# Kernel optimization log

Measured on AMD Instinct MI355X. Metric: run time of the kernel, lower is better.

The kernel has to match this reference:

```python
import jax, jax.numpy as jnp
import numpy as np

H, D_IN, E = 8, 512, 512
KD = VD = E // H  # 64
B, N = 16, 1024  # batch, graph_size (== n_query, self-attention)
NEG_INF = -1e30  # stands in for -np.inf; identical post-softmax, NaN-safe


def _uniform(key, shape, stdv):
    return jax.random.uniform(key, shape, jnp.float32, -stdv, stdv)


def setup_inputs() -> dict:
    key = jax.random.key(0)
    kq, km, k1, k2, k3, k4 = jax.random.split(key, 6)
    q = jax.random.normal(kq, (B, N, D_IN), jnp.float32)
    mask = jax.random.bernoulli(km, 0.15, (B, N, N))
    W_query = _uniform(k1, (H, D_IN, KD), 1.0 / np.sqrt(KD))
    W_key = _uniform(k2, (H, D_IN, KD), 1.0 / np.sqrt(KD))
    W_val = _uniform(k3, (H, D_IN, VD), 1.0 / np.sqrt(VD))
    W_out = _uniform(k4, (H, VD, E), 1.0 / np.sqrt(E))
    return {"q": q, "mask": mask, "W_query": W_query, "W_key": W_key,
            "W_val": W_val, "W_out": W_out}


def reference(q, mask, W_query, W_key, W_val, W_out):
    # h = q (self-attention path of the module)
    kd = W_query.shape[-1]
    scale = 1.0 / np.sqrt(kd).astype(np.float32)
    Q = jnp.einsum('bni,hik->hbnk', q, W_query)   # (H,B,N,kd)
    K = jnp.einsum('bgi,hik->hbgk', q, W_key)     # (H,B,G,kd)
    V = jnp.einsum('bgi,hiv->hbgv', q, W_val)     # (H,B,G,vd)
    compat = scale * jnp.einsum('hbnk,hbgk->hbng', Q, K)  # (H,B,N,G)
    m = mask[None]                                 # (1,B,N,G) broadcasts over heads
    compat = jnp.where(m, NEG_INF, compat)
    attn = jax.nn.softmax(compat, axis=-1)
    attn = jnp.where(m, 0.0, attn)
    heads = jnp.einsum('hbng,hbgv->hbnv', attn, V)
    out = jnp.einsum('hbnv,hve->bne', heads, W_out)  # (B,N,E)
    return out
```

## Files before the change

kernel.cpp:

```cpp
#include <hip/hip_runtime.h>
#include <hip/hip_bf16.h>

#define HH 8
#define DIN 512
#define HD 64
#define BB 16
#define NN 1024
#define LOG2E 1.44269504f

typedef float f32x4 __attribute__((ext_vector_type(4)));
typedef short s16x8 __attribute__((ext_vector_type(8)));
typedef unsigned int u32x4 __attribute__((ext_vector_type(4)));
typedef __bf16 bf16x8 __attribute__((ext_vector_type(8)));

__device__ __forceinline__ short f2bf(float f) {
  union { float f; unsigned u; } v; v.f = f;
  unsigned r = v.u + 0x7FFFu + ((v.u >> 16) & 1u);
  return (short)(r >> 16);
}

__device__ __forceinline__ unsigned cvtpk(float lo, float hi) {
  unsigned r;
  asm("v_cvt_pk_bf16_f32 %0, %1, %2" : "=v"(r) : "v"(lo), "v"(hi));
  return r;
}

__device__ __forceinline__ float exp2v(float x) {
  float r;
  asm("v_exp_f32 %0, %1" : "=v"(r) : "v"(x));
  return r;
}

__device__ __forceinline__ f32x4 mfma16(s16x8 a, s16x8 b, f32x4 c) {
  return __builtin_amdgcn_mfma_f32_16x16x32_bf16(
      __builtin_bit_cast(bf16x8, a), __builtin_bit_cast(bf16x8, b), c, 0, 0, 0);
}

#define GLDS16(gsrc, ldst)                                          \
  __builtin_amdgcn_global_load_lds(                                 \
      (const __attribute__((address_space(1))) void*)(gsrc),        \
      (__attribute__((address_space(3))) void*)(ldst), 16, 0, 0)

__global__ void k_detect(const unsigned char* __restrict__ m, int* __restrict__ flag) {
  const int t = threadIdx.x;
  const int nz = (m[4 * t + 1] != 0);
  unsigned long long b = __ballot(nz);
  __shared__ unsigned int anyv;
  if (t == 0) anyv = 0u;
  __syncthreads();
  if ((t & 63) == 0 && b) atomicOr(&anyv, 1u);
  __syncthreads();
  if (t == 0) flag[0] = (int)anyv;
}

__global__ void k_prep(const void* __restrict__ mk, const int* __restrict__ flag,
                       unsigned char* __restrict__ mwords,
                       const float* __restrict__ q, short* __restrict__ qbf,
                       const float* __restrict__ Wq, const float* __restrict__ Wk,
                       const float* __restrict__ Wv, const float* __restrict__ Wo,
                       short* __restrict__ Wt, short* __restrict__ Wot) {
  __shared__ float t[64][65];
  const int blk = blockIdx.x;
  if (blk < 8192) {
    const int i = blk * 256 + threadIdx.x;
    unsigned bits = 0;
    if (flag[0]) {
      const unsigned long long v = ((const unsigned long long*)mk)[i];
#pragma unroll
      for (int j = 0; j < 8; ++j)
        bits |= (((v >> (8 * j)) & 0xFFull) ? 1u : 0u) << j;
    } else {
      const uint4 a = ((const uint4*)mk)[2 * i];
      const uint4 c = ((const uint4*)mk)[2 * i + 1];
      bits = (a.x ? 1u : 0u) | (a.y ? 2u : 0u) | (a.z ? 4u : 0u) | (a.w ? 8u : 0u) |
             (c.x ? 16u : 0u) | (c.y ? 32u : 0u) | (c.z ? 64u : 0u) | (c.w ? 128u : 0u);
    }
    mwords[i] = (unsigned char)bits;
  } else if (blk < 12288) {
    const int i = (blk - 8192) * 256 + threadIdx.x;
    const float4* s4 = (const float4*)q;
    float4 a = s4[2 * i], c = s4[2 * i + 1];
    s16x8 o;
    o[0] = f2bf(a.x); o[1] = f2bf(a.y); o[2] = f2bf(a.z); o[3] = f2bf(a.w);
    o[4] = f2bf(c.x); o[5] = f2bf(c.y); o[6] = f2bf(c.z); o[7] = f2bf(c.w);
    ((s16x8*)qbf)[i] = o;
  } else {
    const int idx = blk - 12288;
    const float* in;
    short* op;
    int N, k0, n0;
    float scale = 1.0f;
    if (idx < 192) {
      const int mat = idx >> 6, rem = idx & 63, head = rem >> 3, kb = rem & 7;
      in = (mat == 0 ? Wq : (mat == 1 ? Wk : Wv)) + head * (DIN * HD);
      op = Wt + (size_t)(mat * 8 + head) * (HD * DIN);
      N = 64; k0 = kb * 64; n0 = 0;
      if (mat == 0) scale = 0.125f * LOG2E;
    } else {
      const int t2 = idx - 192;
      in = Wo; op = Wot;
      N = 512; k0 = (t2 >> 3) * 64; n0 = (t2 & 7) * 64;
    }
    const int tx = threadIdx.x & 63, ty = threadIdx.x >> 6;
#pragma unroll
    for (int i = 0; i < 16; ++i) {
      const int k = ty + i * 4;
      t[k][tx] = in[(size_t)(k0 + k) * N + n0 + tx];
    }
    __syncthreads();
#pragma unroll
    for (int i = 0; i < 16; ++i) {
      const int n = ty + i * 4;
      op[(size_t)(n0 + n) * DIN + k0 + tx] = f2bf(t[tx][n] * scale);
    }
  }
}

template <int MODE>
__global__ __launch_bounds__(256, 2) void k_gemm(
    const short* __restrict__ Abf, const short* __restrict__ Bmat,
    short* __restrict__ Qb, short* __restrict__ Kb, short* __restrict__ VtG,
    float* __restrict__ out) {
  __shared__ short lds[4 * 128 * 64];
  const int tid = threadIdx.x;
  const int m0 = blockIdx.x * 128, n0 = blockIdx.y * 128;
  const int w = tid >> 6, l = tid & 63;
  const int wm = w >> 1, wn = w & 1;
  const int rowf = l & 15, kg = l >> 4;
  const int srow = l >> 3;
  const int cc = (l & 7) ^ srow;
  const bool isV = (MODE == 0) && (n0 >= 1024);

  f32x4 acc[4][4];
#pragma unroll
  for (int i = 0; i < 4; ++i)
#pragma unroll
    for (int j = 0; j < 4; ++j) acc[i][j] = (f32x4){0.f, 0.f, 0.f, 0.f};

  auto issue = [&](int kt, int bsel) {
    short* base = lds + bsel * 16384;
#pragma unroll
    for (int i = 0; i < 4; ++i) {
      const int row = w * 32 + i * 8;
      GLDS16(Abf + ((size_t)(m0 + row + srow) * 512 + kt * 64 + cc * 8),
             base + row * 64);
      GLDS16(Bmat + ((size_t)(n0 + row + srow) * 512 + kt * 64 + cc * 8),
             base + 8192 + row * 64);
    }
  };
  auto compute = [&](int bsel) {
    short* bA = lds + bsel * 16384;
    short* bB = bA + 8192;
#pragma unroll
    for (int kk = 0; kk < 2; ++kk) {
      s16x8 af[4], bf[4];
#pragma unroll
      for (int i = 0; i < 4; ++i) {
        const int arow = wm * 64 + i * 16 + rowf;
        af[i] = *(const s16x8*)&bA[arow * 64 + (((kk * 4 + kg) ^ (arow & 7)) * 8)];
        const int brow = wn * 64 + i * 16 + rowf;
        bf[i] = *(const s16x8*)&bB[brow * 64 + (((kk * 4 + kg) ^ (brow & 7)) * 8)];
      }
      if (isV) {
#pragma unroll
        for (int i = 0; i < 4; ++i)
#pragma unroll
          for (int j = 0; j < 4; ++j) acc[i][j] = mfma16(bf[j], af[i], acc[i][j]);
      } else {
#pragma unroll
        for (int i = 0; i < 4; ++i)
#pragma unroll
          for (int j = 0; j < 4; ++j) acc[i][j] = mfma16(af[i], bf[j], acc[i][j]);
      }
    }
  };

  issue(0, 0);
  issue(1, 1);
#pragma unroll 1
  for (int kt = 0; kt < 7; ++kt) {
    asm volatile("s_waitcnt vmcnt(8)" ::: "memory");
    __builtin_amdgcn_sched_barrier(0);
    __builtin_amdgcn_s_barrier();
    compute(kt & 1);
    __builtin_amdgcn_s_barrier();
    __builtin_amdgcn_sched_barrier(0);
    if (kt + 2 < 8) issue(kt + 2, kt & 1);
  }
  asm volatile("s_waitcnt vmcnt(0)" ::: "memory");
  __builtin_amdgcn_sched_barrier(0);
  __builtin_amdgcn_s_barrier();
  compute(1);

  if (MODE == 1) {
#pragma unroll
    for (int i = 0; i < 4; ++i)
#pragma unroll
      for (int j = 0; j < 4; ++j)
#pragma unroll
        for (int r = 0; r < 4; ++r) {
          const int m = m0 + wm * 64 + i * 16 + kg * 4 + r;
          const int n = n0 + wn * 64 + j * 16 + rowf;
          out[(size_t)m * DIN + n] = acc[i][j][r];
        }
  } else if (isV) {
    const int bconst = m0 >> 10;
#pragma unroll
    for (int i = 0; i < 4; ++i)
#pragma unroll
      for (int j = 0; j < 4; ++j)
#pragma unroll
        for (int r = 0; r < 4; ++r) {
          const int ng = n0 + wn * 64 + j * 16 + kg * 4 + r;
          const int head = (ng >> 6) & 7, d = ng & 63;
          const int m = m0 + wm * 64 + i * 16 + rowf;
          const int seq = m & 1023;
          VtG[((size_t)(head * BB + bconst) * HD + d) * NN + seq] = f2bf(acc[i][j][r]);
        }
  } else {
#pragma unroll
    for (int i = 0; i < 4; ++i)
#pragma unroll
      for (int j = 0; j < 4; ++j)
#pragma unroll
        for (int r = 0; r < 4; ++r) {
          const int m = m0 + wm * 64 + i * 16 + kg * 4 + r;
          const int ng = n0 + wn * 64 + j * 16 + rowf;
          const int mat = ng >> 9, head = (ng >> 6) & 7, d = ng & 63;
          short* Ob = (mat == 0 ? Qb : Kb) + head * (BB * NN * HD);
          Ob[(size_t)m * HD + d] = f2bf(acc[i][j][r]);
        }
  }
}

__global__ __launch_bounds__(512, 4) void k_attn(
    const short* __restrict__ Qb, const short* __restrict__ Kb, const short* __restrict__ VtG,
    const unsigned int* __restrict__ mw, short* __restrict__ heads) {
  __shared__ short smem[2 * 8192];
  const int tid = threadIdx.x;
  const int w = tid >> 6, l = tid & 63, rowf = l & 15, kg = l >> 4;
  const int r7 = rowf & 7;
  const int lin = blockIdx.x;
  const int gi = (lin >> 3) + ((lin & 7) << 6);
  const int qblk = gi & 3, bh = gi >> 2;
  const int b = bh & 15, h = bh >> 4;
  const int hb = (h * BB + b) * NN;
  const short* Qp = Qb + (size_t)hb * HD;
  const short* Kp = Kb + (size_t)hb * HD;
  const short* Vtp = VtG + (size_t)(h * BB + b) * HD * NN;
  const int wq = qblk * 256 + w * 32;

  s16x8 bQ[2][2];
#pragma unroll
  for (int qi = 0; qi < 2; ++qi)
#pragma unroll
    for (int kk = 0; kk < 2; ++kk)
      bQ[qi][kk] = *(const s16x8*)&Qp[(wq + qi * 16 + rowf) * HD + kk * 32 + kg * 8];

  const f32x4 cW = (f32x4){-24.f, -24.f, -24.f, -24.f};
  f32x4 accO[2][4], accSum[2];
#pragma unroll
  for (int qi = 0; qi < 2; ++qi) {
    accSum[qi] = (f32x4){0.f, 0.f, 0.f, 0.f};
#pragma unroll
    for (int vj = 0; vj < 4; ++vj) accO[qi][vj] = (f32x4){0.f, 0.f, 0.f, 0.f};
  }
  s16x8 aOnes;
#pragma unroll
  for (int jj = 0; jj < 8; ++jj) aOnes[jj] = (short)0x3F80;

  const int kr = tid >> 3, c = tid & 7;
  const int mK = ((kr >> 5) << 1) | ((kr >> 2) & 1);
  const int iK = (((kr >> 3) & 3) << 2) | (kr & 3);
  const int RK = mK * 16 + iK;
  const int dK = RK * 64 + ((c ^ (RK & 7)) * 8);
  const int dV = 4096 + kr * 64 + ((c ^ (kr & 7)) * 8);

  s16x8 rk = *(const s16x8*)&Kp[kr * HD + c * 8];
  s16x8 rv = *(const s16x8*)&Vtp[(size_t)kr * NN + c * 8];
  *(s16x8*)&smem[dK] = rk;
  *(s16x8*)&smem[dV] = rv;
  rk = *(const s16x8*)&Kp[(64 + kr) * HD + c * 8];
  rv = *(const s16x8*)&Vtp[(size_t)kr * NN + 64 + c * 8];

  const unsigned int* mrow0 = mw + (size_t)(b * NN + wq + rowf) * 32;

  int cur = 0;
  for (int kt = 0; kt < NN / 64; ++kt) {
    __syncthreads();
    short* bK = smem + cur * 8192;
    short* bV = bK + 4096;
    if (kt + 1 < NN / 64) {
      short* oB = smem + (cur ^ 1) * 8192;
      *(s16x8*)&oB[dK] = rk;
      *(s16x8*)&oB[dV] = rv;
      if (kt + 2 < NN / 64) {
        const int kn = (kt + 2) * 64;
        rk = *(const s16x8*)&Kp[(kn + kr) * HD + c * 8];
        rv = *(const s16x8*)&Vtp[(size_t)kr * NN + kn + c * 8];
      }
    }

    f32x4 accS[2][4];
    __builtin_amdgcn_s_setprio(1);
#pragma unroll
    for (int m = 0; m < 4; ++m) {
      const int R = m * 16 + rowf;
      s16x8 a0 = *(const s16x8*)&bK[R * 64 + ((kg ^ r7) * 8)];
      s16x8 a1 = *(const s16x8*)&bK[R * 64 + (((4 + kg) ^ r7) * 8)];
      accS[0][m] = mfma16(a0, bQ[0][0], cW);
      accS[0][m] = mfma16(a1, bQ[0][1], accS[0][m]);
      accS[1][m] = mfma16(a0, bQ[1][0], cW);
      accS[1][m] = mfma16(a1, bQ[1][1], accS[1][m]);
    }
    __builtin_amdgcn_s_setprio(0);

    u32x4 pw[2][2];
#pragma unroll
    for (int qi = 0; qi < 2; ++qi) {
      const uint2 mv = *(const uint2*)(mrow0 + qi * 512 + kt * 2);
      const unsigned u0 = mv.x >> (kg * 8);
      const unsigned u1 = mv.y >> (kg * 8);
#pragma unroll
      for (int half = 0; half < 2; ++half) {
        const unsigned u = half ? u1 : u0;
        u32x4 wd;
#pragma unroll
        for (int t = 0; t < 4; ++t) {
          const int j0 = 2 * t, j1 = 2 * t + 1;
          const float e0 = ((u >> j0) & 1u) ? 0.f
                           : exp2v(accS[qi][half * 2 + (j0 >> 2)][j0 & 3]);
          const float e1 = ((u >> j1) & 1u) ? 0.f
                           : exp2v(accS[qi][half * 2 + (j1 >> 2)][j1 & 3]);
          wd[t] = cvtpk(e0, e1);
        }
        pw[qi][half] = wd;
      }
    }

    __builtin_amdgcn_s_setprio(1);
#pragma unroll
    for (int kk = 0; kk < 2; ++kk) {
      const s16x8 pa0 = __builtin_bit_cast(s16x8, pw[0][kk]);
      const s16x8 pa1 = __builtin_bit_cast(s16x8, pw[1][kk]);
      accSum[0] = mfma16(aOnes, pa0, accSum[0]);
      accSum[1] = mfma16(aOnes, pa1, accSum[1]);
#pragma unroll
      for (int vj = 0; vj < 4; ++vj) {
        const int d = vj * 16 + rowf;
        s16x8 aV = *(const s16x8*)&bV[d * 64 + (((kk * 4 + kg) ^ r7) * 8)];
        accO[0][vj] = mfma16(aV, pa0, accO[0][vj]);
        accO[1][vj] = mfma16(aV, pa1, accO[1][vj]);
      }
    }
    __builtin_amdgcn_s_setprio(0);
    cur ^= 1;
  }

  __syncthreads();
  short* tb = smem + w * 2048;
  {
    const float rc0 = 1.0f / accSum[0][0], rc1 = 1.0f / accSum[1][0];
#pragma unroll
    for (int qi = 0; qi < 2; ++qi) {
      const float rc = qi ? rc1 : rc0;
      const int row = qi * 16 + rowf;
#pragma unroll
      for (int vj = 0; vj < 4; ++vj)
#pragma unroll
        for (int r = 0; r < 4; ++r) {
          const int col = vj * 16 + kg * 4 + r;
          tb[row * 64 + (((col >> 3) ^ (row & 7)) * 8) + (col & 7)] =
              f2bf(accO[qi][vj][r] * rc);
        }
    }
  }
#pragma unroll
  for (int it = 0; it < 4; ++it) {
    const int ql = (l >> 3) + it * 8, oct = l & 7;
    s16x8 v = *(const s16x8*)&tb[ql * 64 + ((oct ^ (ql & 7)) * 8)];
    *(s16x8*)&heads[((size_t)(b * NN + wq + ql) * HH + h) * HD + oct * 8] = v;
  }
}

extern "C" void kernel_launch(void* const* d_in, const int* in_sizes, int n_in,
                              void* d_out, int out_size, void* d_ws, size_t ws_size,
                              hipStream_t stream) {
  if (n_in < 6) return;
  const float* q  = (const float*)d_in[0];
  const void*  mk = d_in[1];
  const float* Wq = (const float*)d_in[2];
  const float* Wk = (const float*)d_in[3];
  const float* Wv = (const float*)d_in[4];
  const float* Wo = (const float*)d_in[5];
  float* out = (float*)d_out;

  char* ws = (char*)d_ws;
  size_t o = 0;
  auto alloc = [&](size_t sz) { char* p = ws + o; o = (o + sz + 255) & ~(size_t)255; return p; };
  int*           flag   = (int*)alloc(4);
  unsigned char* mwords = (unsigned char*)alloc((size_t)BB * NN * NN / 8);
  short* qbf   = (short*)alloc((size_t)BB * NN * DIN * 2);
  short* Wt    = (short*)alloc((size_t)3 * HH * HD * DIN * 2);
  short* Wot   = (short*)alloc((size_t)DIN * DIN * 2);
  short* Qbuf  = (short*)alloc((size_t)HH * BB * NN * HD * 2);
  short* Kbuf  = (short*)alloc((size_t)HH * BB * NN * HD * 2);
  short* VtBuf = (short*)alloc((size_t)HH * BB * HD * NN * 2);
  short* heads = (short*)alloc((size_t)BB * NN * HH * HD * 2);
  if (o > ws_size) return;

  k_detect<<<1, 256, 0, stream>>>((const unsigned char*)mk, flag);
  k_prep<<<12544, 256, 0, stream>>>(mk, flag, mwords, q, qbf, Wq, Wk, Wv, Wo, Wt, Wot);
  k_gemm<0><<<dim3(BB * NN / 128, 12), 256, 0, stream>>>(
      qbf, Wt, Qbuf, Kbuf, VtBuf, nullptr);
  k_attn<<<dim3(512), 512, 0, stream>>>(Qbuf, Kbuf, VtBuf,
                                        (const unsigned int*)mwords, heads);
  k_gemm<1><<<dim3(BB * NN / 128, 4), 256, 0, stream>>>(
      heads, Wot, nullptr, nullptr, nullptr, out);
}
```

Before: 118.3 us.

## Stream K/V tiles with direct global-to-LDS loads and interleave softmax with PV MFMAs

Measured after the change: 119.9 us. Within noise of the previous version (+1.3%).

```diff
diff --git a/kernel.cpp b/kernel.cpp
--- a/kernel.cpp
+++ b/kernel.cpp
@@ -269,37 +269,29 @@
 #pragma unroll
   for (int jj = 0; jj < 8; ++jj) aOnes[jj] = (short)0x3F80;
 
-  const int kr = tid >> 3, c = tid & 7;
-  const int mK = ((kr >> 5) << 1) | ((kr >> 2) & 1);
-  const int iK = (((kr >> 3) & 3) << 2) | (kr & 3);
-  const int RK = mK * 16 + iK;
-  const int dK = RK * 64 + ((c ^ (RK & 7)) * 8);
-  const int dV = 4096 + kr * 64 + ((c ^ (kr & 7)) * 8);
-
-  s16x8 rk = *(const s16x8*)&Kp[kr * HD + c * 8];
-  s16x8 rv = *(const s16x8*)&Vtp[(size_t)kr * NN + c * 8];
-  *(s16x8*)&smem[dK] = rk;
-  *(s16x8*)&smem[dV] = rv;
-  rk = *(const s16x8*)&Kp[(64 + kr) * HD + c * 8];
-  rv = *(const s16x8*)&Vtp[(size_t)kr * NN + 64 + c * 8];
+  const int Rs = w * 8 + (l >> 3), cp = l & 7;
+  const int im = Rs >> 4, ii = Rs & 15;
+  const int keyRs = (im >> 1) * 32 + ((ii >> 2) & 3) * 8 + (im & 1) * 4 + (ii & 3);
+  const short* srcK = Kp + keyRs * HD + ((cp ^ (Rs & 7)) * 8);
+  const short* srcV = Vtp + (size_t)Rs * NN + ((cp ^ (Rs & 7)) * 8);
+
+  auto issueT = [&](int t) {
+    short* base = smem + (t & 1) * 8192;
+    GLDS16(srcK + (size_t)t * 64 * HD, base + w * 512);
+    GLDS16(srcV + t * 64, base + 4096 + w * 512);
+  };
 
   const unsigned int* mrow0 = mw + (size_t)(b * NN + wq + rowf) * 32;
 
-  int cur = 0;
+  issueT(0);
+#pragma unroll 1
   for (int kt = 0; kt < NN / 64; ++kt) {
-    __syncthreads();
-    short* bK = smem + cur * 8192;
+    asm volatile("s_waitcnt vmcnt(0)" ::: "memory");
+    __builtin_amdgcn_sched_barrier(0);
+    __builtin_amdgcn_s_barrier();
+    if (kt + 1 < NN / 64) issueT(kt + 1);
+    short* bK = smem + (kt & 1) * 8192;
     short* bV = bK + 4096;
-    if (kt + 1 < NN / 64) {
-      short* oB = smem + (cur ^ 1) * 8192;
-      *(s16x8*)&oB[dK] = rk;
-      *(s16x8*)&oB[dV] = rv;
-      if (kt + 2 < NN / 64) {
-        const int kn = (kt + 2) * 64;
-        rk = *(const s16x8*)&Kp[(kn + kr) * HD + c * 8];
-        rv = *(const s16x8*)&Vtp[(size_t)kr * NN + kn + c * 8];
-      }
-    }
 
     f32x4 accS[2][4];
     __builtin_amdgcn_s_setprio(1);
@@ -315,12 +307,12 @@
     }
     __builtin_amdgcn_s_setprio(0);
 
-    u32x4 pw[2][2];
 #pragma unroll
     for (int qi = 0; qi < 2; ++qi) {
       const uint2 mv = *(const uint2*)(mrow0 + qi * 512 + kt * 2);
       const unsigned u0 = mv.x >> (kg * 8);
       const unsigned u1 = mv.y >> (kg * 8);
+      u32x4 pw[2];
 #pragma unroll
       for (int half = 0; half < 2; ++half) {
         const unsigned u = half ? u1 : u0;
@@ -334,27 +326,22 @@
                            : exp2v(accS[qi][half * 2 + (j1 >> 2)][j1 & 3]);
           wd[t] = cvtpk(e0, e1);
         }
-        pw[qi][half] = wd;
+        pw[half] = wd;
       }
-    }
-
-    __builtin_amdgcn_s_setprio(1);
-#pragma unroll
-    for (int kk = 0; kk < 2; ++kk) {
-      const s16x8 pa0 = __builtin_bit_cast(s16x8, pw[0][kk]);
-      const s16x8 pa1 = __builtin_bit_cast(s16x8, pw[1][kk]);
-      accSum[0] = mfma16(aOnes, pa0, accSum[0]);
-      accSum[1] = mfma16(aOnes, pa1, accSum[1]);
-#pragma unroll
-      for (int vj = 0; vj < 4; ++vj) {
-        const int d = vj * 16 + rowf;
-        s16x8 aV = *(const s16x8*)&bV[d * 64 + (((kk * 4 + kg) ^ r7) * 8)];
-        accO[0][vj] = mfma16(aV, pa0, accO[0][vj]);
-        accO[1][vj] = mfma16(aV, pa1, accO[1][vj]);
+      __builtin_amdgcn_s_setprio(1);
+#pragma unroll
+      for (int kk = 0; kk < 2; ++kk) {
+        const s16x8 pa = __builtin_bit_cast(s16x8, pw[kk]);
+        accSum[qi] = mfma16(aOnes, pa, accSum[qi]);
+#pragma unroll
+        for (int vj = 0; vj < 4; ++vj) {
+          const int d = vj * 16 + rowf;
+          s16x8 aV = *(const s16x8*)&bV[d * 64 + (((kk * 4 + kg) ^ r7) * 8)];
+          accO[qi][vj] = mfma16(aV, pa, accO[qi][vj]);
+        }
       }
-    }
-    __builtin_amdgcn_s_setprio(0);
-    cur ^= 1;
+      __builtin_amdgcn_s_setprio(0);
+    }
   }
 
   __syncthreads();
```
